# Optimization experiments

Hardware: AMD Instinct MI355X
Metric: run time of the kernel (lower is better)

Reference implementation:

```python
import jax, jax.numpy as jnp
import numpy as np

D_MODEL, D_STATE, D_CONV, EXPAND = 512, 16, 4, 2
D_INNER = EXPAND * D_MODEL
DT_RANK = D_MODEL // 16
B, N = 4, 576


def layernorm(x, g, b, eps=1e-5):
    m = x.mean(-1, keepdims=True)
    v = jnp.mean((x - m) ** 2, axis=-1, keepdims=True)
    return (x - m) / jnp.sqrt(v + eps) * g + b


def selective_scan(u, dt, A, Bm, Cm, Dp):
    # u, dt: (B,N,di); Bm,Cm: (B,N,ds); A: (di,ds); Dp: (di,)
    dA = jnp.exp(dt[..., None] * A)                      # (B,N,di,ds)
    dBu = dt[..., None] * Bm[:, :, None, :] * u[..., None]

    def step(h, inp):
        dA_t, dBu_t, C_t = inp                            # (B,di,ds),(B,di,ds),(B,ds)
        h = dA_t * h + dBu_t
        y = jnp.einsum('bds,bs->bd', h, C_t)
        return h, y

    h0 = jnp.zeros((u.shape[0], u.shape[2], A.shape[1]), u.dtype)
    _, ys = jax.lax.scan(step, h0, (dA.transpose(1, 0, 2, 3),
                                    dBu.transpose(1, 0, 2, 3),
                                    Cm.transpose(1, 0, 2)))
    return ys.transpose(1, 0, 2) + u * Dp


def mamba(x, Win, convw, convb, Wx, Wdt, bdt, Alog, Dp, Wout):
    xz = jnp.einsum('bnd,ed->bne', x, Win)                # (B,N,2*di)
    u, z = jnp.split(xz, 2, axis=-1)
    k = convw.shape[1]
    # depthwise causal conv1d
    uc = jax.lax.conv_general_dilated(u.transpose(0, 2, 1), convw[:, None, :],
                                      (1,), [(k - 1, 0)],
                                      feature_group_count=convw.shape[0])
    u = jax.nn.silu((uc + convb[None, :, None]).transpose(0, 2, 1))
    x_dbl = jnp.einsum('bnd,ed->bne', u, Wx)              # (B,N,dt_rank+2*ds)
    ds = Alog.shape[1]
    dt, Bm, Cm = jnp.split(x_dbl, [DT_RANK, DT_RANK + ds], axis=-1)
    dt = jax.nn.softplus(jnp.einsum('bnr,dr->bnd', dt, Wdt) + bdt)
    A = -jnp.exp(Alog)
    y = selective_scan(u, dt, A, Bm, Cm, Dp)
    y = y * jax.nn.silu(z)
    return jnp.einsum('bnd,ed->bne', y, Wout)


def setup_inputs() -> dict:
    key = jax.random.key(0)
    ks = iter(jax.random.split(key, 40))
    s = 0.02
    def rn(shape, scale=s):
        return jax.random.normal(next(ks), shape, jnp.float32) * scale
    inp = {
        'x': jax.random.normal(next(ks), (B, N, D_MODEL), jnp.float32),
        'g1': jnp.ones((D_MODEL,), jnp.float32), 'b1': jnp.zeros((D_MODEL,), jnp.float32),
        'g2': jnp.ones((D_MODEL,), jnp.float32), 'b2': jnp.zeros((D_MODEL,), jnp.float32),
        'merge_W': rn((D_MODEL, 2 * D_MODEL)), 'merge_b': jnp.zeros((D_MODEL,), jnp.float32),
        'ffn_W1': rn((4 * D_MODEL, D_MODEL)), 'ffn_b1': jnp.zeros((4 * D_MODEL,), jnp.float32),
        'ffn_W2': rn((D_MODEL, 4 * D_MODEL)), 'ffn_b2': jnp.zeros((D_MODEL,), jnp.float32),
    }
    for p in ('f_', 'r_'):
        inp[p + 'Win'] = rn((2 * D_INNER, D_MODEL))
        inp[p + 'convw'] = rn((D_INNER, D_CONV), 0.1)
        inp[p + 'convb'] = jnp.zeros((D_INNER,), jnp.float32)
        inp[p + 'Wx'] = rn((DT_RANK + 2 * D_STATE, D_INNER))
        inp[p + 'Wdt'] = rn((D_INNER, DT_RANK), 0.1)
        inp[p + 'bdt'] = jnp.zeros((D_INNER,), jnp.float32)
        inp[p + 'Alog'] = jnp.log(jnp.broadcast_to(jnp.arange(1, D_STATE + 1, dtype=jnp.float32), (D_INNER, D_STATE)))
        inp[p + 'D'] = jnp.ones((D_INNER,), jnp.float32)
        inp[p + 'Wout'] = rn((D_MODEL, D_INNER))
    return inp


def reference(x, g1, b1, g2, b2,
              f_Win, f_convw, f_convb, f_Wx, f_Wdt, f_bdt, f_Alog, f_D, f_Wout,
              r_Win, r_convw, r_convb, r_Wx, r_Wdt, r_bdt, r_Alog, r_D, r_Wout,
              merge_W, merge_b, ffn_W1, ffn_b1, ffn_W2, ffn_b2):
    residual = x
    xn = layernorm(x, g1, b1)
    xf = mamba(xn, f_Win, f_convw, f_convb, f_Wx, f_Wdt, f_bdt, f_Alog, f_D, f_Wout)
    xb = mamba(jnp.flip(xn, axis=1), r_Win, r_convw, r_convb, r_Wx, r_Wdt, r_bdt, r_Alog, r_D, r_Wout)
    xb = jnp.flip(xb, axis=1)
    xm = jnp.concatenate([xf, xb], axis=-1)
    xm = jnp.einsum('bne,de->bnd', xm, merge_W) + merge_b
    x = residual + xm  # dropout is identity in eval mode
    residual = x
    xn = layernorm(x, g2, b2)
    h = jax.nn.gelu(jnp.einsum('bnd,ed->bne', xn, ffn_W1) + ffn_b1)
    h = jnp.einsum('bne,de->bnd', h, ffn_W2) + ffn_b2
    return residual + h
```

## Files before the change

### kernel.cpp

```cpp
#include <hip/hip_runtime.h>
#include <hip/hip_bf16.h>
#include <math.h>

#define D_MODEL 512
#define D_STATE 16
#define D_CONV  4
#define D_INNER 1024
#define DT_RANK 32
#define BB      4
#define NN      576
#define TOK     (BB*NN)
#define NCHUNK  6
#define CLEN    (NN/NCHUNK)

__device__ __forceinline__ float fexp(float x)  { return __expf(x); }
__device__ __forceinline__ float fsilu(float x) { return x / (1.f + __expf(-x)); }
__device__ __forceinline__ float fsoftplus(float x) {
    return fmaxf(x, 0.f) + __logf(1.f + __expf(-fabsf(x)));
}
__device__ __forceinline__ float fgelu(float u) {
    float a = 0.7978845608028654f * (u + 0.044715f * u * u * u);
    float t = 1.f - 2.f / (1.f + __expf(2.f * a));
    return 0.5f * u * (1.f + t);
}

__global__ __launch_bounds__(64) void ln_kernel(const float* __restrict__ x,
                                                const float* __restrict__ g,
                                                const float* __restrict__ b,
                                                float* __restrict__ o) {
    int t = blockIdx.x;
    int lane = threadIdx.x;
    const float* xr = x + (size_t)t * D_MODEL;
    float4 v0 = ((const float4*)xr)[lane];
    float4 v1 = ((const float4*)xr)[64 + lane];
    float s = v0.x + v0.y + v0.z + v0.w + v1.x + v1.y + v1.z + v1.w;
    #pragma unroll
    for (int m = 32; m; m >>= 1) s += __shfl_xor(s, m);
    float mean = s * (1.0f / D_MODEL);
    float dx[8] = {v0.x-mean, v0.y-mean, v0.z-mean, v0.w-mean,
                   v1.x-mean, v1.y-mean, v1.z-mean, v1.w-mean};
    float q = 0.f;
    #pragma unroll
    for (int i = 0; i < 8; i++) q += dx[i]*dx[i];
    #pragma unroll
    for (int m = 32; m; m >>= 1) q += __shfl_xor(q, m);
    float rstd = rsqrtf(q * (1.0f / D_MODEL) + 1e-5f);
    float4 g0 = ((const float4*)g)[lane], g1 = ((const float4*)g)[64 + lane];
    float4 b0 = ((const float4*)b)[lane], b1 = ((const float4*)b)[64 + lane];
    float4 o0, o1;
    o0.x = dx[0]*rstd*g0.x + b0.x; o0.y = dx[1]*rstd*g0.y + b0.y;
    o0.z = dx[2]*rstd*g0.z + b0.z; o0.w = dx[3]*rstd*g0.w + b0.w;
    o1.x = dx[4]*rstd*g1.x + b1.x; o1.y = dx[5]*rstd*g1.y + b1.y;
    o1.z = dx[6]*rstd*g1.z + b1.z; o1.w = dx[7]*rstd*g1.w + b1.w;
    float* orow = o + (size_t)t * D_MODEL;
    ((float4*)orow)[lane] = o0;
    ((float4*)orow)[64 + lane] = o1;
}

#define EP_NONE     0
#define EP_SOFTPLUS 1
#define EP_GELU     2
#define EP_BIAS_ADD 3

typedef __attribute__((ext_vector_type(8))) short bf16x8;
typedef __attribute__((ext_vector_type(4))) float f32x4;

__device__ __forceinline__ void split8(float4 q0, float4 q1,
                                       uint4 &hi, uint4 &lo) {
    float f[8] = {q0.x, q0.y, q0.z, q0.w, q1.x, q1.y, q1.z, q1.w};
    unsigned hb[8], lb[8];
    #pragma unroll
    for (int i = 0; i < 8; i++) {
        unsigned u = __float_as_uint(f[i]);
        unsigned r = (u + 0x7FFFu + ((u >> 16) & 1u)) >> 16;
        hb[i] = r & 0xFFFFu;
        float lf = f[i] - __uint_as_float(r << 16);
        unsigned ul = __float_as_uint(lf);
        lb[i] = ((ul + 0x7FFFu + ((ul >> 16) & 1u)) >> 16) & 0xFFFFu;
    }
    hi = make_uint4(hb[0]|(hb[1]<<16), hb[2]|(hb[3]<<16),
                    hb[4]|(hb[5]<<16), hb[6]|(hb[7]<<16));
    lo = make_uint4(lb[0]|(lb[1]<<16), lb[2]|(lb[3]<<16),
                    lb[4]|(lb[5]<<16), lb[6]|(lb[7]<<16));
}

template<int EP>
__global__ __launch_bounds__(256) void gemm_mfma(
        const float* __restrict__ A, int lda,
        const float* __restrict__ W,
        float* __restrict__ C, int ldc,
        const float* __restrict__ bias,
        const float* __restrict__ add, int ldadd,
        int N, int K) {
    __shared__ short AsH[64][40], AsL[64][40], BsH[64][40], BsL[64][40];
    int tid  = threadIdx.x;
    int lane = tid & 63;
    int wave = tid >> 6;
    int wm = wave >> 1, wn = wave & 1;
    int m0 = blockIdx.y * 64, n0 = blockIdx.x * 64;
    int srow = tid >> 2;
    int skb  = (tid & 3) * 8;

    f32x4 acc[2][2] = {};

    for (int k0 = 0; k0 < K; k0 += 32) {
        float4 a0 = *(const float4*)&A[(size_t)(m0 + srow) * lda + k0 + skb];
        float4 a1 = *(const float4*)&A[(size_t)(m0 + srow) * lda + k0 + skb + 4];
        float4 w0 = *(const float4*)&W[(size_t)(n0 + srow) * K + k0 + skb];
        float4 w1 = *(const float4*)&W[(size_t)(n0 + srow) * K + k0 + skb + 4];
        uint4 ah, al, bh, bl;
        split8(a0, a1, ah, al);
        split8(w0, w1, bh, bl);
        __syncthreads();
        *(uint4*)&AsH[srow][skb] = ah;
        *(uint4*)&AsL[srow][skb] = al;
        *(uint4*)&BsH[srow][skb] = bh;
        *(uint4*)&BsL[srow][skb] = bl;
        __syncthreads();

        int hk = (lane >> 4) * 8;
        int rr = lane & 15;
        bf16x8 fAh[2], fAl[2], fBh[2], fBl[2];
        #pragma unroll
        for (int mi = 0; mi < 2; mi++) {
            int r = wm * 32 + mi * 16 + rr;
            fAh[mi] = *(const bf16x8*)&AsH[r][hk];
            fAl[mi] = *(const bf16x8*)&AsL[r][hk];
        }
        #pragma unroll
        for (int ni = 0; ni < 2; ni++) {
            int c = wn * 32 + ni * 16 + rr;
            fBh[ni] = *(const bf16x8*)&BsH[c][hk];
            fBl[ni] = *(const bf16x8*)&BsL[c][hk];
        }
        #pragma unroll
        for (int mi = 0; mi < 2; mi++)
            #pragma unroll
            for (int ni = 0; ni < 2; ni++) {
                acc[mi][ni] = __builtin_amdgcn_mfma_f32_16x16x32_bf16(
                    fAh[mi], fBh[ni], acc[mi][ni], 0, 0, 0);
                acc[mi][ni] = __builtin_amdgcn_mfma_f32_16x16x32_bf16(
                    fAh[mi], fBl[ni], acc[mi][ni], 0, 0, 0);
                acc[mi][ni] = __builtin_amdgcn_mfma_f32_16x16x32_bf16(
                    fAl[mi], fBh[ni], acc[mi][ni], 0, 0, 0);
            }
    }

    #pragma unroll
    for (int mi = 0; mi < 2; mi++) {
        #pragma unroll
        for (int ni = 0; ni < 2; ni++) {
            int r0 = m0 + wm * 32 + mi * 16 + (lane >> 4) * 4;
            int c  = n0 + wn * 32 + ni * 16 + (lane & 15);
            #pragma unroll
            for (int j = 0; j < 4; j++) {
                float v = acc[mi][ni][j];
                if (EP == EP_GELU) {
                    v = fgelu(v + bias[c]);
                } else if (EP == EP_BIAS_ADD) {
                    v += bias[c];
                    v += add[(size_t)(r0 + j) * ldadd + c];
                }
                C[(size_t)(r0 + j) * ldc + c] = v;
            }
        }
    }
}

template<int EP>
__global__ __launch_bounds__(256) void gemm_nt(
        const float* __restrict__ A, int lda,
        const float* __restrict__ W,
        float* __restrict__ C, int ldc,
        const float* __restrict__ bias,
        const float* __restrict__ add, int ldadd,
        int M, int N, int K) {
    __shared__ float As[32][68];
    __shared__ float Bs[32][68];
    int tid = threadIdx.x;
    int tx = tid & 15, ty = tid >> 4;
    int m0 = blockIdx.y * 64, n0 = blockIdx.x * 64;
    int arow = tid >> 3;
    int acol = (tid & 7) * 4;
    float acc[4][4] = {};

    for (int k0 = 0; k0 < K; k0 += 32) {
        float4 a0 = *(const float4*)&A[(size_t)(m0 + arow) * lda + k0 + acol];
        float4 a1 = *(const float4*)&A[(size_t)(m0 + arow + 32) * lda + k0 + acol];
        float4 w0 = *(const float4*)&W[(size_t)(n0 + arow) * K + k0 + acol];
        float4 w1 = *(const float4*)&W[(size_t)(n0 + arow + 32) * K + k0 + acol];
        __syncthreads();
        As[acol + 0][arow] = a0.x; As[acol + 1][arow] = a0.y;
        As[acol + 2][arow] = a0.z; As[acol + 3][arow] = a0.w;
        As[acol + 0][arow + 32] = a1.x; As[acol + 1][arow + 32] = a1.y;
        As[acol + 2][arow + 32] = a1.z; As[acol + 3][arow + 32] = a1.w;
        Bs[acol + 0][arow] = w0.x; Bs[acol + 1][arow] = w0.y;
        Bs[acol + 2][arow] = w0.z; Bs[acol + 3][arow] = w0.w;
        Bs[acol + 0][arow + 32] = w1.x; Bs[acol + 1][arow + 32] = w1.y;
        Bs[acol + 2][arow + 32] = w1.z; Bs[acol + 3][arow + 32] = w1.w;
        __syncthreads();
        #pragma unroll
        for (int kk = 0; kk < 32; kk++) {
            float av[4], bv[4];
            *(float4*)&av[0] = *(const float4*)&As[kk][ty * 4];
            *(float4*)&bv[0] = *(const float4*)&Bs[kk][tx * 4];
            #pragma unroll
            for (int i = 0; i < 4; i++)
                #pragma unroll
                for (int j = 0; j < 4; j++)
                    acc[i][j] = fmaf(av[i], bv[j], acc[i][j]);
        }
    }

    int mbase = m0 + ty * 4, nbase = n0 + tx * 4;
    #pragma unroll
    for (int i = 0; i < 4; i++) {
        float vv[4];
        #pragma unroll
        for (int j = 0; j < 4; j++) {
            float v = acc[i][j];
            if (EP == EP_SOFTPLUS) {
                v = fsoftplus(v + bias[nbase + j]);
            } else if (EP == EP_GELU) {
                v = fgelu(v + bias[nbase + j]);
            } else if (EP == EP_BIAS_ADD) {
                v += bias[nbase + j];
                v += add[(size_t)(mbase + i) * ldadd + nbase + j];
            }
            vv[j] = v;
        }
        *(float4*)&C[(size_t)(mbase + i) * ldc + nbase] =
            make_float4(vv[0], vv[1], vv[2], vv[3]);
    }
}

__global__ __launch_bounds__(256) void gemm_wx_splitk(
        const float* __restrict__ A,
        const float* __restrict__ W,
        float* __restrict__ Cpart) {
    __shared__ float As[32][68];
    __shared__ float Bs[32][68];
    int tid = threadIdx.x;
    int tx = tid & 15, ty = tid >> 4;
    int m0 = blockIdx.y * 64;
    int z = blockIdx.z;
    const float* Az = A + z * 256;
    const float* Wz = W + z * 256;
    int arow = tid >> 3;
    int acol = (tid & 7) * 4;
    float acc[4][4] = {};

    for (int k0 = 0; k0 < 256; k0 += 32) {
        float4 a0 = *(const float4*)&Az[(size_t)(m0 + arow) * 1024 + k0 + acol];
        float4 a1 = *(const float4*)&Az[(size_t)(m0 + arow + 32) * 1024 + k0 + acol];
        float4 w0 = *(const float4*)&Wz[(size_t)(arow) * 1024 + k0 + acol];
        float4 w1 = *(const float4*)&Wz[(size_t)(arow + 32) * 1024 + k0 + acol];
        __syncthreads();
        As[acol + 0][arow] = a0.x; As[acol + 1][arow] = a0.y;
        As[acol + 2][arow] = a0.z; As[acol + 3][arow] = a0.w;
        As[acol + 0][arow + 32] = a1.x; As[acol + 1][arow + 32] = a1.y;
        As[acol + 2][arow + 32] = a1.z; As[acol + 3][arow + 32] = a1.w;
        Bs[acol + 0][arow] = w0.x; Bs[acol + 1][arow] = w0.y;
        Bs[acol + 2][arow] = w0.z; Bs[acol + 3][arow] = w0.w;
        Bs[acol + 0][arow + 32] = w1.x; Bs[acol + 1][arow + 32] = w1.y;
        Bs[acol + 2][arow + 32] = w1.z; Bs[acol + 3][arow + 32] = w1.w;
        __syncthreads();
        #pragma unroll
        for (int kk = 0; kk < 32; kk++) {
            float av[4], bv[4];
            *(float4*)&av[0] = *(const float4*)&As[kk][ty * 4];
            *(float4*)&bv[0] = *(const float4*)&Bs[kk][tx * 4];
            #pragma unroll
            for (int i = 0; i < 4; i++)
                #pragma unroll
                for (int j = 0; j < 4; j++)
                    acc[i][j] = fmaf(av[i], bv[j], acc[i][j]);
        }
    }

    float* Cz = Cpart + (size_t)z * TOK * 64;
    int mbase = m0 + ty * 4, nbase = tx * 4;
    #pragma unroll
    for (int i = 0; i < 4; i++)
        *(float4*)&Cz[(size_t)(mbase + i) * 64 + nbase] =
            make_float4(acc[i][0], acc[i][1], acc[i][2], acc[i][3]);
}

__global__ __launch_bounds__(256) void reduce4_kernel(
        const float* __restrict__ Cpart, float* __restrict__ xd) {
    int i = blockIdx.x * 256 + threadIdx.x;
    const int M64 = TOK * 64;
    xd[i] = Cpart[i] + Cpart[M64 + i] + Cpart[2 * M64 + i] + Cpart[3 * M64 + i];
}

__global__ __launch_bounds__(256) void conv_silu_kernel(
        const float* __restrict__ xz, const float* __restrict__ w,
        const float* __restrict__ cb, float* __restrict__ out, int dir) {
    int idx = blockIdx.x * 256 + threadIdx.x;
    int c = idx & (D_INNER - 1);
    int t = idx >> 10;
    int b = t / NN, n = t % NN;
    const float* up = xz + (size_t)b * NN * (2 * D_INNER) + c;
    float4 wv = *(const float4*)&w[c * 4];
    float acc;
    if (dir == 0) {
        acc =                 up[(size_t)n * (2*D_INNER)] * wv.w;
        if (n >= 1) acc = fmaf(up[(size_t)(n-1) * (2*D_INNER)], wv.z, acc);
        if (n >= 2) acc = fmaf(up[(size_t)(n-2) * (2*D_INNER)], wv.y, acc);
        if (n >= 3) acc = fmaf(up[(size_t)(n-3) * (2*D_INNER)], wv.x, acc);
    } else {
        acc =                    up[(size_t)n * (2*D_INNER)] * wv.w;
        if (n+1 < NN) acc = fmaf(up[(size_t)(n+1) * (2*D_INNER)], wv.z, acc);
        if (n+2 < NN) acc = fmaf(up[(size_t)(n+2) * (2*D_INNER)], wv.y, acc);
        if (n+3 < NN) acc = fmaf(up[(size_t)(n+3) * (2*D_INNER)], wv.x, acc);
    }
    out[(size_t)t * D_INNER + c] = fsilu(acc + cb[c]);
}

__global__ __launch_bounds__(256) void scan_pass1(
        const float* __restrict__ dt, const float* __restrict__ xdbl,
        const float* __restrict__ u, const float* __restrict__ Alog,
        float* __restrict__ hend, float* __restrict__ prodA, int dir) {
    int lane = threadIdx.x & 63;
    int wave = threadIdx.x >> 6;
    int w = blockIdx.x * 4 + wave;
    int s = lane & 15;
    int dl = lane >> 4;
    int dg = w & 255;
    int b  = (w >> 8) & 3;
    int c  = w >> 10;
    int d = dg * 4 + dl;
    float A_ds = -fexp(Alog[d * D_STATE + s]);
    float h = 0.f, P = 1.f;
    const int UF = 16;
    for (int i0 = c * CLEN; i0 < (c + 1) * CLEN; i0 += UF) {
        float dtv[UF], uv[UF], Bv[UF];
        #pragma unroll
        for (int j = 0; j < UF; j++) {
            int i = i0 + j;
            int n = dir ? (NN - 1 - i) : i;
            size_t tt = (size_t)b * NN + n;
            dtv[j] = dt[tt * D_INNER + d];
            uv[j]  = u[tt * D_INNER + d];
            Bv[j]  = xdbl[tt * 64 + 32 + s];
        }
        #pragma unroll
        for (int j = 0; j < UF; j++) {
            float a = fexp(dtv[j] * A_ds);
            h = fmaf(a, h, dtv[j] * Bv[j] * uv[j]);
            P *= a;
        }
    }
    int idx = ((c * 4 + b) * 1024 + d) * 16 + s;
    hend[idx] = h;
    prodA[idx] = P;
}

__global__ __launch_bounds__(256) void scan_combine(
        const float* __restrict__ hend, const float* __restrict__ prodA,
        float* __restrict__ hin) {
    int e = blockIdx.x * 256 + threadIdx.x;
    float run = 0.f;
    #pragma unroll
    for (int c = 0; c < NCHUNK; c++) {
        hin[c * 65536 + e] = run;
        run = fmaf(prodA[c * 65536 + e], run, hend[c * 65536 + e]);
    }
}

__global__ __launch_bounds__(256) void scan_pass2(
        const float* __restrict__ dt, const float* __restrict__ xdbl,
        const float* __restrict__ u, const float* __restrict__ xz,
        const float* __restrict__ Alog, const float* __restrict__ Dp,
        const float* __restrict__ hin, float* __restrict__ y, int dir) {
    int lane = threadIdx.x & 63;
    int wave = threadIdx.x >> 6;
    int w = blockIdx.x * 4 + wave;
    int s = lane & 15;
    int dl = lane >> 4;
    int dg = w & 255;
    int b  = (w >> 8) & 3;
    int c  = w >> 10;
    int d = dg * 4 + dl;
    float A_ds = -fexp(Alog[d * D_STATE + s]);
    float Dd = Dp[d];
    float h = hin[((c * 4 + b) * 1024 + d) * 16 + s];
    const int UF = 16;
    for (int i0 = c * CLEN; i0 < (c + 1) * CLEN; i0 += UF) {
        float dtv[UF], uv[UF], Bv[UF], Cv[UF];
        #pragma unroll
        for (int j = 0; j < UF; j++) {
            int i = i0 + j;
            int n = dir ? (NN - 1 - i) : i;
            size_t tt = (size_t)b * NN + n;
            dtv[j] = dt[tt * D_INNER + d];
            uv[j]  = u[tt * D_INNER + d];
            Bv[j]  = xdbl[tt * 64 + 32 + s];
            Cv[j]  = xdbl[tt * 64 + 48 + s];
        }
        float p[UF];
        #pragma unroll
        for (int j = 0; j < UF; j++) {
            float a = fexp(dtv[j] * A_ds);
            h = fmaf(a, h, dtv[j] * Bv[j] * uv[j]);
            p[j] = h * Cv[j];
        }
        #pragma unroll
        for (int j = 0; j < UF; j++) {
            p[j] += __shfl_xor(p[j], 1);
            p[j] += __shfl_xor(p[j], 2);
            p[j] += __shfl_xor(p[j], 4);
            p[j] += __shfl_xor(p[j], 8);
        }
        if (s == 0) {
            #pragma unroll
            for (int j = 0; j < UF; j++) {
                int i = i0 + j;
                int n = dir ? (NN - 1 - i) : i;
                size_t tt = (size_t)b * NN + n;
                float zv = xz[tt * (2 * D_INNER) + D_INNER + d];
                float yv = p[j] + uv[j] * Dd;
                yv *= fsilu(zv);
                y[tt * D_INNER + d] = yv;
            }
        }
    }
}

extern "C" void kernel_launch(void* const* d_in, const int* in_sizes, int n_in,
                              void* d_out, int out_size, void* d_ws, size_t ws_size,
                              hipStream_t stream) {
    const float* x       = (const float*)d_in[0];
    const float* g1      = (const float*)d_in[1];
    const float* b1      = (const float*)d_in[2];
    const float* g2      = (const float*)d_in[3];
    const float* b2      = (const float*)d_in[4];
    const float* merge_W = (const float*)d_in[5];
    const float* merge_b = (const float*)d_in[6];
    const float* ffn_W1  = (const float*)d_in[7];
    const float* ffn_b1  = (const float*)d_in[8];
    const float* ffn_W2  = (const float*)d_in[9];
    const float* ffn_b2  = (const float*)d_in[10];
    const float* Win[2]   = {(const float*)d_in[11], (const float*)d_in[20]};
    const float* convw[2] = {(const float*)d_in[12], (const float*)d_in[21]};
    const float* convb[2] = {(const float*)d_in[13], (const float*)d_in[22]};
    const float* Wx[2]    = {(const float*)d_in[14], (const float*)d_in[23]};
    const float* Wdt[2]   = {(const float*)d_in[15], (const float*)d_in[24]};
    const float* bdt[2]   = {(const float*)d_in[16], (const float*)d_in[25]};
    const float* Alog[2]  = {(const float*)d_in[17], (const float*)d_in[26]};
    const float* Dp[2]    = {(const float*)d_in[18], (const float*)d_in[27]};
    const float* Wout[2]  = {(const float*)d_in[19], (const float*)d_in[28]};
    float* out = (float*)d_out;

    float* ws = (float*)d_ws;
    const size_t T = TOK;
    float* xn  = ws;
    float* xz  = xn  + T * 512;
    float* uc  = xz  + T * 2048;
    float* xd  = uc  + T * 1024;
    float* dt  = xd  + T * 64;
    float* xfb = dt  + T * 1024;
    float* x2  = xfb + T * 1024;
    float* xd4   = x2;
    float* hendb = x2;
    float* prodb = x2 + (size_t)NCHUNK * 65536;
    float* hinb  = x2 + (size_t)2 * NCHUNK * 65536;

    ln_kernel<<<TOK, 64, 0, stream>>>(x, g1, b1, xn);

    for (int p = 0; p < 2; p++) {
        gemm_mfma<EP_NONE><<<dim3(2048/64, TOK/64), 256, 0, stream>>>(
            xn, 512, Win[p], xz, 2048, nullptr, nullptr, 0, 2048, 512);
        conv_silu_kernel<<<TOK * D_INNER / 256, 256, 0, stream>>>(
            xz, convw[p], convb[p], uc, p);
        gemm_wx_splitk<<<dim3(1, TOK/64, 4), 256, 0, stream>>>(uc, Wx[p], xd4);
        reduce4_kernel<<<TOK * 64 / 256, 256, 0, stream>>>(xd4, xd);
        gemm_nt<EP_SOFTPLUS><<<dim3(1024/64, TOK/64), 256, 0, stream>>>(
            xd, 64, Wdt[p], dt, 1024, bdt[p], nullptr, 0, TOK, 1024, 32);
        scan_pass1<<<NCHUNK * 256, 256, 0, stream>>>(
            dt, xd, uc, Alog[p], hendb, prodb, p);
        scan_combine<<<256, 256, 0, stream>>>(hendb, prodb, hinb);
        scan_pass2<<<NCHUNK * 256, 256, 0, stream>>>(
            dt, xd, uc, xz, Alog[p], Dp[p], hinb, uc, p);
        gemm_mfma<EP_NONE><<<dim3(512/64, TOK/64), 256, 0, stream>>>(
            uc, 1024, Wout[p], xfb + p * 512, 1024, nullptr, nullptr, 0, 512, 1024);
    }

    gemm_mfma<EP_BIAS_ADD><<<dim3(512/64, TOK/64), 256, 0, stream>>>(
        xfb, 1024, merge_W, x2, 512, merge_b, x, 512, 512, 1024);

    ln_kernel<<<TOK, 64, 0, stream>>>(x2, g2, b2, xn);

    gemm_mfma<EP_GELU><<<dim3(2048/64, TOK/64), 256, 0, stream>>>(
        xn, 512, ffn_W1, xz, 2048, ffn_b1, nullptr, 0, 2048, 512);

    gemm_mfma<EP_BIAS_ADD><<<dim3(512/64, TOK/64), 256, 0, stream>>>(
        xz, 2048, ffn_W2, out, 512, ffn_b2, x2, 512, 512, 2048);
}
```

Measured before the change: 595.0 us.

## Prefetch next GEMM K-tile into registers, truncate bf16 split, pad LDS rows

The MFMA GEMM main loop now loads the next K-tile from global memory into registers right after the shared-memory store, so the loads overlap with the MFMA work on the current tile. The bf16 hi/lo split switches from round-to-nearest to truncation, with the low part absorbing the residual, which removes several integer ops per element. The LDS row stride changes from 40 to 44 shorts to alter the bank-conflict pattern. Truncating the hi part leaves a slightly larger remainder in the low part, which can reduce accuracy. Register prefetching also raises register pressure.

```diff
diff --git a/kernel.cpp b/kernel.cpp
--- a/kernel.cpp
+++ b/kernel.cpp
@@ -65,24 +65,24 @@
 typedef __attribute__((ext_vector_type(8))) short bf16x8;
 typedef __attribute__((ext_vector_type(4))) float f32x4;
 
-__device__ __forceinline__ void split8(float4 q0, float4 q1,
-                                       uint4 &hi, uint4 &lo) {
+__device__ __forceinline__ void split8t(float4 q0, float4 q1,
+                                        uint4 &hi, uint4 &lo) {
     float f[8] = {q0.x, q0.y, q0.z, q0.w, q1.x, q1.y, q1.z, q1.w};
-    unsigned hb[8], lb[8];
+    unsigned hu[8], lu[8];
     #pragma unroll
     for (int i = 0; i < 8; i++) {
         unsigned u = __float_as_uint(f[i]);
-        unsigned r = (u + 0x7FFFu + ((u >> 16) & 1u)) >> 16;
-        hb[i] = r & 0xFFFFu;
-        float lf = f[i] - __uint_as_float(r << 16);
-        unsigned ul = __float_as_uint(lf);
-        lb[i] = ((ul + 0x7FFFu + ((ul >> 16) & 1u)) >> 16) & 0xFFFFu;
-    }
-    hi = make_uint4(hb[0]|(hb[1]<<16), hb[2]|(hb[3]<<16),
-                    hb[4]|(hb[5]<<16), hb[6]|(hb[7]<<16));
-    lo = make_uint4(lb[0]|(lb[1]<<16), lb[2]|(lb[3]<<16),
-                    lb[4]|(lb[5]<<16), lb[6]|(lb[7]<<16));
-}
+        hu[i] = u & 0xFFFF0000u;
+        float lf = f[i] - __uint_as_float(hu[i]);
+        lu[i] = __float_as_uint(lf) & 0xFFFF0000u;
+    }
+    hi = make_uint4((hu[0] >> 16) | hu[1], (hu[2] >> 16) | hu[3],
+                    (hu[4] >> 16) | hu[5], (hu[6] >> 16) | hu[7]);
+    lo = make_uint4((lu[0] >> 16) | lu[1], (lu[2] >> 16) | lu[3],
+                    (lu[4] >> 16) | lu[5], (lu[6] >> 16) | lu[7]);
+}
+
+#define LDSW 44
 
 template<int EP>
 __global__ __launch_bounds__(256) void gemm_mfma(
@@ -92,7 +92,7 @@
         const float* __restrict__ bias,
         const float* __restrict__ add, int ldadd,
         int N, int K) {
-    __shared__ short AsH[64][40], AsL[64][40], BsH[64][40], BsL[64][40];
+    __shared__ short AsH[64][LDSW], AsL[64][LDSW], BsH[64][LDSW], BsL[64][LDSW];
     int tid  = threadIdx.x;
     int lane = tid & 63;
     int wave = tid >> 6;
@@ -103,20 +103,30 @@
 
     f32x4 acc[2][2] = {};
 
+    const float* pA = &A[(size_t)(m0 + srow) * lda + skb];
+    const float* pW = &W[(size_t)(n0 + srow) * K + skb];
+    float4 a0 = *(const float4*)(pA);
+    float4 a1 = *(const float4*)(pA + 4);
+    float4 w0 = *(const float4*)(pW);
+    float4 w1 = *(const float4*)(pW + 4);
+
     for (int k0 = 0; k0 < K; k0 += 32) {
-        float4 a0 = *(const float4*)&A[(size_t)(m0 + srow) * lda + k0 + skb];
-        float4 a1 = *(const float4*)&A[(size_t)(m0 + srow) * lda + k0 + skb + 4];
-        float4 w0 = *(const float4*)&W[(size_t)(n0 + srow) * K + k0 + skb];
-        float4 w1 = *(const float4*)&W[(size_t)(n0 + srow) * K + k0 + skb + 4];
         uint4 ah, al, bh, bl;
-        split8(a0, a1, ah, al);
-        split8(w0, w1, bh, bl);
+        split8t(a0, a1, ah, al);
+        split8t(w0, w1, bh, bl);
         __syncthreads();
         *(uint4*)&AsH[srow][skb] = ah;
         *(uint4*)&AsL[srow][skb] = al;
         *(uint4*)&BsH[srow][skb] = bh;
         *(uint4*)&BsL[srow][skb] = bl;
         __syncthreads();
+
+        if (k0 + 32 < K) {
+            a0 = *(const float4*)(pA + k0 + 32);
+            a1 = *(const float4*)(pA + k0 + 36);
+            w0 = *(const float4*)(pW + k0 + 32);
+            w1 = *(const float4*)(pW + k0 + 36);
+        }
 
         int hk = (lane >> 4) * 8;
         int rr = lane & 15;
```

Measured after the change: 554.0 us. 1.07x faster.
